# Kernel tuning notes

Hardware: AMD Instinct MI355X
Metric: run time of the kernel (lower is better)

Reference implementation:

```python
import jax, jax.numpy as jnp
import numpy as np

N_NODES = 100000
N_EDGES = 1600000
C_IN = 500
HIDDEN = 256
C_OUT = 50
K = 10
K_HALF = K // 2  # 5
ALPHA = 0.1


def _prop(x, src, dst, norm, n):
    # one propagate(): gather source features, scale by edge norm, scatter-add to dst
    msg = norm[:, None] * x[src]          # [E, F]
    return jax.ops.segment_sum(msg, dst, num_segments=n)


def setup_inputs() -> dict:
    key = jax.random.key(0)
    k0, k1, k2, k3 = jax.random.split(key, 4)
    x = jax.random.normal(k0, (N_NODES, C_IN), dtype=jnp.float32)
    edge_index = jax.random.randint(k1, (2, N_EDGES), 0, N_NODES, dtype=jnp.int32)
    # temp[k] = alpha * (1-alpha)^(2k), k = 0..K//2  (even-order PPR coefficients)
    temp = jnp.asarray(ALPHA * (1.0 - ALPHA) ** (2 * np.arange(K_HALF + 1)), dtype=jnp.float32)
    W1 = jax.random.normal(k2, (C_IN, HIDDEN), dtype=jnp.float32) / np.sqrt(C_IN).astype(np.float32)
    b1 = jnp.zeros((HIDDEN,), jnp.float32)
    W2 = jax.random.normal(k3, (HIDDEN, C_OUT), dtype=jnp.float32) / np.sqrt(HIDDEN).astype(np.float32)
    b2 = jnp.zeros((C_OUT,), jnp.float32)
    return {"x": x, "edge_index": edge_index, "W1": W1, "b1": b1, "W2": W2, "b2": b2, "temp": temp}


def reference(x, edge_index, W1, b1, W2, b2, temp):
    n = x.shape[0]
    src, dst = edge_index[0], edge_index[1]
    # sym-normalized adjacency A_hat = D^-1/2 A D^-1/2.
    # (get_laplacian 'sym' then add_self_loops(-norm, 1.0): the -1/+1 diagonal
    #  entries cancel under scatter-add, leaving exactly A_hat.)
    deg = jax.ops.segment_sum(jnp.ones_like(src, dtype=x.dtype), src, num_segments=n)
    dinv = jnp.where(deg > 0, jax.lax.rsqrt(jnp.maximum(deg, 1e-12)), 0.0)
    norm = dinv[src] * dinv[dst]          # [E]

    # MLP (dropout is identity in eval mode)
    h = jax.nn.relu(x @ W1 + b1)
    h = h @ W2 + b2                        # [N, C_OUT]

    hidden0 = h * temp[0]

    def body(k, carry):
        xk, hid = carry
        xk = _prop(xk, src, dst, norm, n)  # A_hat @ x
        xk = _prop(xk, src, dst, norm, n)  # A_hat^2 @ x
        hid = hid + temp[k + 1] * xk
        return (xk, hid)

    _, hidden = jax.lax.fori_loop(0, K_HALF, body, (h, hidden0))
    return jax.nn.log_softmax(hidden, axis=1)
```

## Files before the change

### kernel.cpp

```cpp
#include <hip/hip_runtime.h>

#define NN 100000
#define CIN 500
#define KPAD 512
#define HID 256
#define COUT 50
#define NPADOUT 64
#define FPAD 64

#define NBLK 256
#define CB 128
#define NC ((NN + CB - 1) / CB)
#define NCB (NC * NBLK)
#define NCB2 (2 * NCB)

typedef __attribute__((ext_vector_type(8))) short short8;
typedef __attribute__((ext_vector_type(4))) float f32x4;

static __device__ __forceinline__ unsigned short f2bf(float f) {
  union { float f; unsigned u; } v; v.f = f;
  unsigned r = (v.u + 0x7fffu + ((v.u >> 16) & 1u)) >> 16;
  return (unsigned short)r;
}

static __device__ __forceinline__ int slotAt(const int* __restrict__ incl,
                                             const int* __restrict__ bpre, int g) {
  return g ? incl[g - 1] + bpre[(g - 1) >> 10] : 0;
}


__launch_bounds__(256)
__global__ void k_p1(const int* __restrict__ src, const int* __restrict__ dst,
                     int* __restrict__ blk_cnt, int E, int chunk) {
  __shared__ int bd[NC], bs[NC];
  int tid = threadIdx.x;
  for (int i = tid; i < NC; i += 256) { bd[i] = 0; bs[i] = 0; }
  __syncthreads();
  int e0 = blockIdx.x * chunk, e1 = min(E, e0 + chunk);
  for (int e = e0 + tid; e < e1; e += 256) {
    atomicAdd(&bd[dst[e] >> 7], 1);
    atomicAdd(&bs[src[e] >> 7], 1);
  }
  __syncthreads();
  for (int i = tid; i < NC; i += 256) {
    blk_cnt[i * NBLK + blockIdx.x] = bd[i];
    blk_cnt[NCB + i * NBLK + blockIdx.x] = bs[i];
  }
}


__global__ void k_scan_a(const int* __restrict__ hist, int* __restrict__ incl,
                         int* __restrict__ bsum, int n) {
  __shared__ int ts[256];
  int tid = threadIdx.x;
  int base = blockIdx.x * 1024 + tid * 4;
  int a0 = 0, a1 = 0, a2 = 0, a3 = 0;
  if (base + 3 < n) {
    a0 = hist[base]; a1 = hist[base + 1]; a2 = hist[base + 2]; a3 = hist[base + 3];
  } else {
    if (base     < n) a0 = hist[base];
    if (base + 1 < n) a1 = hist[base + 1];
    if (base + 2 < n) a2 = hist[base + 2];
    if (base + 3 < n) a3 = hist[base + 3];
  }
  a1 += a0; a2 += a1; a3 += a2;
  ts[tid] = a3;
  __syncthreads();
  for (int o = 1; o < 256; o <<= 1) {
    int v = ts[tid];
    if (tid >= o) v += ts[tid - o];
    __syncthreads();
    ts[tid] = v;
    __syncthreads();
  }
  int ex = tid ? ts[tid - 1] : 0;
  if (base     < n) incl[base]     = a0 + ex;
  if (base + 1 < n) incl[base + 1] = a1 + ex;
  if (base + 2 < n) incl[base + 2] = a2 + ex;
  if (base + 3 < n) incl[base + 3] = a3 + ex;
  if (tid == 255) bsum[blockIdx.x] = ts[255];
}

__global__ void k_scan_b(const int* __restrict__ bsum, int* __restrict__ bpre, int nb) {
  __shared__ int s[512];
  int tid = threadIdx.x;
  s[tid] = (tid < nb) ? bsum[tid] : 0;
  __syncthreads();
  for (int o = 1; o < 512; o <<= 1) {
    int v = s[tid];
    if (tid >= o) v += s[tid - o];
    __syncthreads();
    s[tid] = v;
    __syncthreads();
  }
  if (tid < nb) bpre[tid] = tid ? s[tid - 1] : 0;
}


__launch_bounds__(256)
__global__ void k_p2(const int* __restrict__ src, const int* __restrict__ dst,
                     const int* __restrict__ incl, const int* __restrict__ bpre,
                     int* __restrict__ pkd, unsigned char* __restrict__ pks, int E, int chunk) {
  __shared__ int cd[NC], cs[NC];
  int tid = threadIdx.x;
  for (int i = tid; i < NC; i += 256) {
    cd[i] = slotAt(incl, bpre, i * NBLK + blockIdx.x);
    cs[i] = slotAt(incl, bpre, NCB + i * NBLK + blockIdx.x) - E;
  }
  __syncthreads();
  int e0 = blockIdx.x * chunk, e1 = min(E, e0 + chunk);
  for (int e = e0 + tid; e < e1; e += 256) {
    int s = src[e], d = dst[e];
    int pd = atomicAdd(&cd[d >> 7], 1);
    pkd[pd] = (s << 7) | (d & 127);
    int ps = atomicAdd(&cs[s >> 7], 1);
    pks[ps] = (unsigned char)(s & 127);
  }
}


__launch_bounds__(256)
__global__ void k_p3s(const int* __restrict__ incl, const int* __restrict__ bpre,
                      const unsigned char* __restrict__ pks, float* __restrict__ dinv, int E) {
  __shared__ int hist[CB];
  int b = blockIdx.x, tid = threadIdx.x;
  if (tid < CB) hist[tid] = 0;
  __syncthreads();
  int s0 = slotAt(incl, bpre, NCB + b * NBLK) - E;
  int s1 = slotAt(incl, bpre, NCB + (b + 1) * NBLK) - E;
  for (int e = s0 + tid; e < s1; e += 256) atomicAdd(&hist[pks[e]], 1);
  __syncthreads();
  if (tid < CB) {
    int node = b * CB + tid;
    if (node < NN) {
      int c = hist[tid];
      dinv[node] = c > 0 ? rsqrtf((float)c) : 0.f;
    }
  }
}


__launch_bounds__(256)
__global__ void k_p3d(const int* __restrict__ incl, const int* __restrict__ bpre,
                      const int* __restrict__ pkd, const float* __restrict__ dinv,
                      int* __restrict__ offs, int2* __restrict__ epk, int E) {
  __shared__ int hist[CB], base[CB], cur[CB];
  int b = blockIdx.x, tid = threadIdx.x;
  if (tid < CB) hist[tid] = 0;
  __syncthreads();
  int s0 = slotAt(incl, bpre, b * NBLK);
  int s1 = slotAt(incl, bpre, (b + 1) * NBLK);
  for (int e = s0 + tid; e < s1; e += 256) atomicAdd(&hist[pkd[e] & 127], 1);
  __syncthreads();
  if (tid == 0) {
    int acc = s0;
    for (int i = 0; i < CB; i++) { base[i] = acc; cur[i] = acc; acc += hist[i]; }
  }
  __syncthreads();
  if (tid < CB) {
    int node = b * CB + tid;
    if (node < NN) offs[node] = base[tid];
  }
  if (b == gridDim.x - 1 && tid == 0) offs[NN] = E;
  for (int e = s0 + tid; e < s1; e += 256) {
    int pk = pkd[e];
    int fine = pk & 127, s = pk >> 7;
    int pos = atomicAdd(&cur[fine], 1);
    float nm = dinv[s] * dinv[b * CB + fine];
    epk[pos] = make_int2(s, __float_as_int(nm));
  }
}


__global__ void k_wt(const float* __restrict__ W1, const float* __restrict__ W2,
                     unsigned short* __restrict__ W1T, unsigned short* __restrict__ W2T) {
  int idx = blockIdx.x * 256 + threadIdx.x;
  if (idx < HID * KPAD) {
    int n = idx >> 9, k = idx & 511;
    W1T[idx] = (k < CIN) ? f2bf(W1[(long)k * HID + n]) : (unsigned short)0;
  } else if (idx < HID * KPAD + NPADOUT * HID) {
    int i2 = idx - HID * KPAD;
    int n = i2 >> 8, k = i2 & 255;
    W2T[i2] = (n < COUT) ? f2bf(W2[(long)k * COUT + n]) : (unsigned short)0;
  }
}


#define LOADS(ra0_, ra1_, rb0_, rb1_, kkc)                                        \
  {                                                                               \
    const int kk_ = (kkc);                                                        \
    bool okk = kk_ + sc * 4 <= 496;                                               \
    if (okA && okk) ra0_ = *reinterpret_cast<const float4*>(&X[xbaseA + kk_]);    \
    else { ra0_.x = ra0_.y = ra0_.z = ra0_.w = 0.f; }                             \
    if (okB && okk) ra1_ = *reinterpret_cast<const float4*>(&X[xbaseB + kk_]);    \
    else { ra1_.x = ra1_.y = ra1_.z = ra1_.w = 0.f; }                             \
    rb0_ = *reinterpret_cast<const uint4*>(&W1T[wbase0 + kk_]);                   \
    rb1_ = *reinterpret_cast<const uint4*>(&W1T[wbase1 + kk_]);                   \
  }

#define STORE_LDS(As_, Bs_, ra0_, ra1_, rb0_, rb1_)                               \
  {                                                                               \
    ushort4 v0, v1;                                                               \
    v0.x = f2bf(ra0_.x); v0.y = f2bf(ra0_.y); v0.z = f2bf(ra0_.z); v0.w = f2bf(ra0_.w); \
    v1.x = f2bf(ra1_.x); v1.y = f2bf(ra1_.y); v1.z = f2bf(ra1_.z); v1.w = f2bf(ra1_.w); \
    *reinterpret_cast<ushort4*>(&As_[sr * 40 + sc * 4]) = v0;                     \
    *reinterpret_cast<ushort4*>(&As_[(sr + 64) * 40 + sc * 4]) = v1;              \
    *reinterpret_cast<uint4*>(&Bs_[br * 40 + bc * 8]) = rb0_;                     \
    *reinterpret_cast<uint4*>(&Bs_[(br + 128) * 40 + bc * 8]) = rb1_;             \
  }

#define COMPUTE(As_, Bs_)                                                         \
  {                                                                               \
    short8 af[4], bfr[4];                                                         \
    const int koff = (lane >> 4) * 8;                                             \
    _Pragma("unroll")                                                             \
    for (int i = 0; i < 4; i++)                                                   \
      af[i] = *reinterpret_cast<const short8*>(&As_[(wr * 64 + i * 16 + (lane & 15)) * 40 + koff]); \
    _Pragma("unroll")                                                             \
    for (int j = 0; j < 4; j++)                                                   \
      bfr[j] = *reinterpret_cast<const short8*>(&Bs_[(wc * 64 + j * 16 + (lane & 15)) * 40 + koff]); \
    _Pragma("unroll")                                                             \
    for (int i = 0; i < 4; i++)                                                   \
      _Pragma("unroll")                                                           \
      for (int j = 0; j < 4; j++)                                                 \
        acc[i][j] = __builtin_amdgcn_mfma_f32_16x16x32_bf16(af[i], bfr[j], acc[i][j], 0, 0, 0); \
  }

__launch_bounds__(512)
__global__ void k_mlp(const float* __restrict__ X, const unsigned short* __restrict__ W1T,
                      const float* __restrict__ b1, const unsigned short* __restrict__ W2T,
                      const float* __restrict__ b2, unsigned short* __restrict__ X0B) {
  __shared__ unsigned short smem[2 * 15360];
  const int tid = threadIdx.x;
  const int lane = tid & 63, w = tid >> 6;
  const int wr = w >> 2, wc = w & 3;
  const int row0 = blockIdx.x * 128;
  f32x4 acc[4][4] = {};
  const int sr = tid >> 3, sc = tid & 7;
  const int br = tid >> 2, bc = tid & 3;

  float4 raA0, raA1; uint4 rbA0, rbA1;
  float4 raB0, raB1; uint4 rbB0, rbB1;

  const int growA = row0 + sr;
  const int growB = row0 + sr + 64;
  const bool okA = growA < NN, okB = growB < NN;
  const long xbaseA = (long)growA * CIN + sc * 4;
  const long xbaseB = (long)growB * CIN + sc * 4;
  const long wbase0 = (long)br * KPAD + bc * 8;
  const long wbase1 = (long)(br + 128) * KPAD + bc * 8;

  LOADS(raA0, raA1, rbA0, rbA1, 0);
  LOADS(raB0, raB1, rbB0, rbB1, 32);

#pragma unroll
  for (int tt = 0; tt < 8; tt++) {
    const int kk0 = tt * 64;
    {
      unsigned short* As = smem;
      unsigned short* Bs = smem + 128 * 40;
      STORE_LDS(As, Bs, raA0, raA1, rbA0, rbA1);
      __syncthreads();
      if (kk0 + 64 < KPAD) LOADS(raA0, raA1, rbA0, rbA1, kk0 + 64);
      COMPUTE(As, Bs);
    }
    {
      unsigned short* As = smem + 15360;
      unsigned short* Bs = As + 128 * 40;
      STORE_LDS(As, Bs, raB0, raB1, rbB0, rbB1);
      __syncthreads();
      if (kk0 + 96 < KPAD) LOADS(raB0, raB1, rbB0, rbB1, kk0 + 96);
      COMPUTE(As, Bs);
    }
  }

  unsigned short* Hs = smem;
  const int rt = w >> 1;
  const int jh = w & 1;
#pragma unroll
  for (int ph = 0; ph < 2; ph++) {
    __syncthreads();
    if (wr == ph) {
#pragma unroll
      for (int i = 0; i < 4; i++) {
        int lr = i * 16 + (lane >> 4) * 4;
#pragma unroll
        for (int j = 0; j < 4; j++) {
          int col = wc * 64 + j * 16 + (lane & 15);
          float bv = b1[col];
#pragma unroll
          for (int r = 0; r < 4; r++) {
            float v = acc[i][j][r] + bv;
            v = v > 0.f ? v : 0.f;
            Hs[(lr + r) * 264 + col] = f2bf(v);
          }
        }
      }
    }
    __syncthreads();
    f32x4 acc2[2] = {};
    const int koff = (lane >> 4) * 8;
    for (int kk = 0; kk < HID; kk += 32) {
      short8 a = *reinterpret_cast<const short8*>(&Hs[(rt * 16 + (lane & 15)) * 264 + kk + koff]);
#pragma unroll
      for (int jj = 0; jj < 2; jj++) {
        int n = (jh * 2 + jj) * 16 + (lane & 15);
        short8 b = *reinterpret_cast<const short8*>(&W2T[n * HID + kk + koff]);
        acc2[jj] = __builtin_amdgcn_mfma_f32_16x16x32_bf16(a, b, acc2[jj], 0, 0, 0);
      }
    }
#pragma unroll
    for (int jj = 0; jj < 2; jj++) {
      int col = (jh * 2 + jj) * 16 + (lane & 15);
      float bv = (col < COUT) ? b2[col] : 0.f;
#pragma unroll
      for (int r = 0; r < 4; r++) {
        int row = row0 + ph * 64 + rt * 16 + (lane >> 4) * 4 + r;
        if (row < NN) {
          float v = acc2[jj][r] + bv;
          X0B[((long)row << 6) + col] = f2bf(v);
        }
      }
    }
  }
}


__launch_bounds__(256)
__global__ void k_prop(const int* __restrict__ offs, const int2* __restrict__ epk,
                       const unsigned short* __restrict__ xin,
                       unsigned short* __restrict__ xout) {
  const long long* __restrict__ epk8 = reinterpret_cast<const long long*>(epk);
  int node = blockIdx.x * 16 + (threadIdx.x >> 4);
  if (node >= NN) return;
  int h = threadIdx.x & 15;
  int fp = h * 4;
  int s0 = offs[node], s1 = offs[node + 1];
  float a0 = 0.f, a1 = 0.f, a2 = 0.f, a3 = 0.f;
  int e = s0;
  for (; e + 7 < s1; e += 8) {
    long long p[8];
#pragma unroll
    for (int q = 0; q < 8; q++) p[q] = epk8[e + q];
    uint2 v[8];
#pragma unroll
    for (int q = 0; q < 8; q++)
      v[q] = *reinterpret_cast<const uint2*>(&xin[((long)(int)p[q] << 6) + fp]);
#pragma unroll
    for (int q = 0; q < 8; q++) {
      float wq = __int_as_float((int)(p[q] >> 32));
      a0 += wq * __uint_as_float(v[q].x << 16);
      a1 += wq * __uint_as_float(v[q].x & 0xffff0000u);
      a2 += wq * __uint_as_float(v[q].y << 16);
      a3 += wq * __uint_as_float(v[q].y & 0xffff0000u);
    }
  }
  for (; e + 3 < s1; e += 4) {
    long long p0 = epk8[e], p1 = epk8[e + 1], p2 = epk8[e + 2], p3 = epk8[e + 3];
    uint2 v0 = *reinterpret_cast<const uint2*>(&xin[((long)(int)p0 << 6) + fp]);
    uint2 v1 = *reinterpret_cast<const uint2*>(&xin[((long)(int)p1 << 6) + fp]);
    uint2 v2 = *reinterpret_cast<const uint2*>(&xin[((long)(int)p2 << 6) + fp]);
    uint2 v3 = *reinterpret_cast<const uint2*>(&xin[((long)(int)p3 << 6) + fp]);
    float w0 = __int_as_float((int)(p0 >> 32)), w1 = __int_as_float((int)(p1 >> 32));
    float w2 = __int_as_float((int)(p2 >> 32)), w3 = __int_as_float((int)(p3 >> 32));
    a0 += w0 * __uint_as_float(v0.x << 16) + w1 * __uint_as_float(v1.x << 16)
        + w2 * __uint_as_float(v2.x << 16) + w3 * __uint_as_float(v3.x << 16);
    a1 += w0 * __uint_as_float(v0.x & 0xffff0000u) + w1 * __uint_as_float(v1.x & 0xffff0000u)
        + w2 * __uint_as_float(v2.x & 0xffff0000u) + w3 * __uint_as_float(v3.x & 0xffff0000u);
    a2 += w0 * __uint_as_float(v0.y << 16) + w1 * __uint_as_float(v1.y << 16)
        + w2 * __uint_as_float(v2.y << 16) + w3 * __uint_as_float(v3.y << 16);
    a3 += w0 * __uint_as_float(v0.y & 0xffff0000u) + w1 * __uint_as_float(v1.y & 0xffff0000u)
        + w2 * __uint_as_float(v2.y & 0xffff0000u) + w3 * __uint_as_float(v3.y & 0xffff0000u);
  }
  for (; e < s1; e++) {
    long long p0 = epk8[e];
    float w0 = __int_as_float((int)(p0 >> 32));
    uint2 v0 = *reinterpret_cast<const uint2*>(&xin[((long)(int)p0 << 6) + fp]);
    a0 += w0 * __uint_as_float(v0.x << 16);
    a1 += w0 * __uint_as_float(v0.x & 0xffff0000u);
    a2 += w0 * __uint_as_float(v0.y << 16);
    a3 += w0 * __uint_as_float(v0.y & 0xffff0000u);
  }
  unsigned d0 = ((unsigned)f2bf(a1) << 16) | (unsigned)f2bf(a0);
  unsigned d1 = ((unsigned)f2bf(a3) << 16) | (unsigned)f2bf(a2);
  unsigned long long pk8 = ((unsigned long long)d1 << 32) | d0;
  *reinterpret_cast<unsigned long long*>(&xout[((long)node << 6) + fp]) = pk8;
}


__launch_bounds__(256)
__global__ void k_fin(const unsigned short* __restrict__ x0,
                      const unsigned short* __restrict__ x1,
                      const unsigned short* __restrict__ x2,
                      const unsigned short* __restrict__ x3,
                      const unsigned short* __restrict__ x4,
                      const unsigned short* __restrict__ x5,
                      const float* __restrict__ temp, float* __restrict__ out) {
  int node = blockIdx.x * 4 + (threadIdx.x >> 6);
  if (node >= NN) return;
  int f = threadIdx.x & 63;
  float v = -INFINITY;
  if (f < COUT) {
    long idx = ((long)node << 6) + f;
    v = temp[0] * __uint_as_float((unsigned)x0[idx] << 16)
      + temp[1] * __uint_as_float((unsigned)x1[idx] << 16)
      + temp[2] * __uint_as_float((unsigned)x2[idx] << 16)
      + temp[3] * __uint_as_float((unsigned)x3[idx] << 16)
      + temp[4] * __uint_as_float((unsigned)x4[idx] << 16)
      + temp[5] * __uint_as_float((unsigned)x5[idx] << 16);
  }
  float m = v;
#pragma unroll
  for (int o = 32; o > 0; o >>= 1) m = fmaxf(m, __shfl_xor(m, o, 64));
  float ex = (f < COUT) ? expf(v - m) : 0.f;
  float s = ex;
#pragma unroll
  for (int o = 32; o > 0; o >>= 1) s += __shfl_xor(s, o, 64);
  if (f < COUT) out[(long)node * COUT + f] = (v - m) - logf(s);
}


extern "C" void kernel_launch(void* const* d_in, const int* in_sizes, int n_in,
                              void* d_out, int out_size, void* d_ws, size_t ws_size,
                              hipStream_t stream) {
  const float* X  = (const float*)d_in[0];
  const int* EI   = (const int*)d_in[1];
  const float* W1 = (const float*)d_in[2];
  const float* B1 = (const float*)d_in[3];
  const float* W2 = (const float*)d_in[4];
  const float* B2 = (const float*)d_in[5];
  const float* TEMP = (const float*)d_in[6];
  const int E = in_sizes[1] / 2;
  const int* src = EI;
  const int* dst = EI + E;

  char* ws = (char*)d_ws;
  size_t off = 0;
  auto alloc = [&](size_t bytes) -> void* {
    off = (off + 511) & ~(size_t)511;
    void* p = ws + off;
    off += bytes;
    return p;
  };
  unsigned short* W1T = (unsigned short*)alloc((size_t)HID * KPAD * 2);
  unsigned short* W2T = (unsigned short*)alloc((size_t)NPADOUT * HID * 2);
  unsigned short* XB[7];
  for (int i = 0; i < 7; i++) XB[i] = (unsigned short*)alloc((size_t)NN * FPAD * 2);
  float* DINV = (float*)alloc((size_t)NN * 4);
  int* OFFS   = (int*)alloc((size_t)(NN + 1) * 4);
  int* BLKC   = (int*)alloc((size_t)NCB2 * 4);
  int* INCL   = (int*)alloc((size_t)NCB2 * 4);
  int* BSUM   = (int*)alloc(512 * 4);
  int* BPRE   = (int*)alloc(512 * 4);
  int* PKD    = (int*)alloc((size_t)E * 4);
  unsigned char* PKS = (unsigned char*)alloc((size_t)E);
  int2* EPK   = (int2*)alloc((size_t)E * 8);

  const int chunk = (E + NBLK - 1) / NBLK;
  const int nsa = (NCB2 + 1023) / 1024;

  k_p1<<<NBLK, 256, 0, stream>>>(src, dst, BLKC, E, chunk);
  k_scan_a<<<nsa, 256, 0, stream>>>(BLKC, INCL, BSUM, NCB2);
  k_scan_b<<<1, 512, 0, stream>>>(BSUM, BPRE, nsa);
  k_p2<<<NBLK, 256, 0, stream>>>(src, dst, INCL, BPRE, PKD, PKS, E, chunk);
  k_p3s<<<NC, 256, 0, stream>>>(INCL, BPRE, PKS, DINV, E);
  k_p3d<<<NC, 256, 0, stream>>>(INCL, BPRE, PKD, DINV, OFFS, EPK, E);

  k_wt<<<(HID * KPAD + NPADOUT * HID + 255) / 256, 256, 0, stream>>>(W1, W2, W1T, W2T);

  k_mlp<<<(NN + 127) / 128, 512, 0, stream>>>(X, W1T, B1, W2T, B2, XB[0]);

  const int PB = (NN + 15) / 16;
  for (int k = 0; k < 5; k++) {
    k_prop<<<PB, 256, 0, stream>>>(OFFS, EPK, XB[k], XB[6]);
    k_prop<<<PB, 256, 0, stream>>>(OFFS, EPK, XB[6], XB[k + 1]);
  }
  k_fin<<<(NN + 3) / 4, 256, 0, stream>>>(XB[0], XB[1], XB[2], XB[3], XB[4], XB[5],
                                          TEMP, (float*)d_out);
}
```

Before: 790.5 us.

## Pre-convert X to padded bf16 and stream MLP tiles via global_load_lds

Adds a conversion kernel that writes X as a zero-padded bf16 matrix (512 columns, padded rows), then a new MLP kernel that loads A and W1 tiles straight into LDS with global_load_lds before doing MFMA. The goal is to halve the bytes the GEMM reads and drop the register-staged fp32 loads, conversion and LDS stores from the GEMM inner loop. The cost is an extra ~100 MB write and read pass plus workspace space. The new LDS layout has no padding, so LDS bank conflicts are possible. It falls back to the old kernel when the workspace is too small.

```diff
diff --git a/kernel.cpp b/kernel.cpp
--- a/kernel.cpp
+++ b/kernel.cpp
@@ -1,6 +1,7 @@
 #include <hip/hip_runtime.h>
 
 #define NN 100000
+#define NROWP 100096
 #define CIN 500
 #define KPAD 512
 #define HID 256
@@ -182,6 +183,129 @@
     int i2 = idx - HID * KPAD;
     int n = i2 >> 8, k = i2 & 255;
     W2T[i2] = (n < COUT) ? f2bf(W2[(long)k * COUT + n]) : (unsigned short)0;
+  }
+}
+
+
+__launch_bounds__(256)
+__global__ void k_cvt(const float* __restrict__ X, unsigned short* __restrict__ XC) {
+  const long total = (long)NROWP * KPAD;
+  long idx = ((long)blockIdx.x * 256 + threadIdx.x) * 8;
+  const long stride = (long)gridDim.x * 256 * 8;
+  for (; idx < total; idx += stride) {
+    int row = (int)(idx >> 9);
+    int c = (int)(idx & 511);
+    ushort4 o0 = {0, 0, 0, 0}, o1 = {0, 0, 0, 0};
+    if (row < NN && c < CIN) {
+      const float* xp = &X[(long)row * CIN + c];
+      if (c + 8 <= CIN) {
+        float4 f0 = *reinterpret_cast<const float4*>(xp);
+        float4 f1 = *reinterpret_cast<const float4*>(xp + 4);
+        o0.x = f2bf(f0.x); o0.y = f2bf(f0.y); o0.z = f2bf(f0.z); o0.w = f2bf(f0.w);
+        o1.x = f2bf(f1.x); o1.y = f2bf(f1.y); o1.z = f2bf(f1.z); o1.w = f2bf(f1.w);
+      } else {
+        o0.x = f2bf(xp[0]); o0.y = f2bf(xp[1]); o0.z = f2bf(xp[2]); o0.w = f2bf(xp[3]);
+      }
+    }
+    *reinterpret_cast<ushort4*>(&XC[idx]) = o0;
+    *reinterpret_cast<ushort4*>(&XC[idx + 4]) = o1;
+  }
+}
+
+
+__launch_bounds__(512)
+__global__ void k_mlp_lds(const unsigned short* __restrict__ XC,
+                          const unsigned short* __restrict__ W1T,
+                          const float* __restrict__ b1,
+                          const unsigned short* __restrict__ W2T,
+                          const float* __restrict__ b2,
+                          unsigned short* __restrict__ X0B) {
+  __shared__ unsigned short smem[64 * 264];
+  const int tid = threadIdx.x;
+  const int lane = tid & 63, w = tid >> 6;
+  const int wr = w >> 2, wc = w & 3;
+  const int row0 = blockIdx.x * 128;
+  f32x4 acc[4][4] = {};
+
+  const int l2 = lane >> 2, l3 = lane & 3;
+  const unsigned short* gA  = XC  + (((long)(row0 + 16 * w + l2)) << 9) + l3 * 8;
+  const unsigned short* gB0 = W1T + (((long)(32 * w + l2)) << 9) + l3 * 8;
+  const unsigned short* gB1 = W1T + (((long)(32 * w + 16 + l2)) << 9) + l3 * 8;
+  unsigned short* ldsA  = smem + w * 512;
+  unsigned short* ldsB0 = smem + 4096 + 2 * w * 512;
+  unsigned short* ldsB1 = smem + 4096 + (2 * w + 1) * 512;
+
+  for (int kk = 0; kk < KPAD; kk += 32) {
+    __syncthreads();
+    __builtin_amdgcn_global_load_lds((const void*)(gA + kk),  (void*)ldsA,  16, 0, 0);
+    __builtin_amdgcn_global_load_lds((const void*)(gB0 + kk), (void*)ldsB0, 16, 0, 0);
+    __builtin_amdgcn_global_load_lds((const void*)(gB1 + kk), (void*)ldsB1, 16, 0, 0);
+    __syncthreads();
+    short8 af[4], bfr[4];
+    const int koff = (lane >> 4) * 8;
+#pragma unroll
+    for (int i = 0; i < 4; i++)
+      af[i] = *reinterpret_cast<const short8*>(
+          &smem[(wr * 64 + i * 16 + (lane & 15)) * 32 + koff]);
+#pragma unroll
+    for (int j = 0; j < 4; j++)
+      bfr[j] = *reinterpret_cast<const short8*>(
+          &smem[4096 + (wc * 64 + j * 16 + (lane & 15)) * 32 + koff]);
+#pragma unroll
+    for (int i = 0; i < 4; i++)
+#pragma unroll
+      for (int j = 0; j < 4; j++)
+        acc[i][j] = __builtin_amdgcn_mfma_f32_16x16x32_bf16(af[i], bfr[j], acc[i][j], 0, 0, 0);
+  }
+
+  unsigned short* Hs = smem;
+  const int rt = w >> 1;
+  const int jh = w & 1;
+#pragma unroll
+  for (int ph = 0; ph < 2; ph++) {
+    __syncthreads();
+    if (wr == ph) {
+#pragma unroll
+      for (int i = 0; i < 4; i++) {
+        int lr = i * 16 + (lane >> 4) * 4;
+#pragma unroll
+        for (int j = 0; j < 4; j++) {
+          int col = wc * 64 + j * 16 + (lane & 15);
+          float bv = b1[col];
+#pragma unroll
+          for (int r = 0; r < 4; r++) {
+            float v = acc[i][j][r] + bv;
+            v = v > 0.f ? v : 0.f;
+            Hs[(lr + r) * 264 + col] = f2bf(v);
+          }
+        }
+      }
+    }
+    __syncthreads();
+    f32x4 acc2[2] = {};
+    const int koff = (lane >> 4) * 8;
+    for (int kk = 0; kk < HID; kk += 32) {
+      short8 a = *reinterpret_cast<const short8*>(&Hs[(rt * 16 + (lane & 15)) * 264 + kk + koff]);
+#pragma unroll
+      for (int jj = 0; jj < 2; jj++) {
+        int n = (jh * 2 + jj) * 16 + (lane & 15);
+        short8 b = *reinterpret_cast<const short8*>(&W2T[n * HID + kk + koff]);
+        acc2[jj] = __builtin_amdgcn_mfma_f32_16x16x32_bf16(a, b, acc2[jj], 0, 0, 0);
+      }
+    }
+#pragma unroll
+    for (int jj = 0; jj < 2; jj++) {
+      int col = (jh * 2 + jj) * 16 + (lane & 15);
+      float bv = (col < COUT) ? b2[col] : 0.f;
+#pragma unroll
+      for (int r = 0; r < 4; r++) {
+        int row = row0 + ph * 64 + rt * 16 + (lane >> 4) * 4 + r;
+        if (row < NN) {
+          float v = acc2[jj][r] + bv;
+          X0B[((long)row << 6) + col] = f2bf(v);
+        }
+      }
+    }
   }
 }
 
@@ -456,6 +580,13 @@
   unsigned char* PKS = (unsigned char*)alloc((size_t)E);
   int2* EPK   = (int2*)alloc((size_t)E * 8);
 
+  const size_t xc_bytes = (size_t)NROWP * KPAD * 2;
+  unsigned short* XC = nullptr;
+  {
+    size_t need = ((off + 511) & ~(size_t)511) + xc_bytes;
+    if (need <= ws_size) XC = (unsigned short*)alloc(xc_bytes);
+  }
+
   const int chunk = (E + NBLK - 1) / NBLK;
   const int nsa = (NCB2 + 1023) / 1024;
 
@@ -468,7 +599,12 @@
 
   k_wt<<<(HID * KPAD + NPADOUT * HID + 255) / 256, 256, 0, stream>>>(W1, W2, W1T, W2T);
 
-  k_mlp<<<(NN + 127) / 128, 512, 0, stream>>>(X, W1T, B1, W2T, B2, XB[0]);
+  if (XC) {
+    k_cvt<<<2048, 256, 0, stream>>>(X, XC);
+    k_mlp_lds<<<(NN + 127) / 128, 512, 0, stream>>>(XC, W1T, B1, W2T, B2, XB[0]);
+  } else {
+    k_mlp<<<(NN + 127) / 128, 512, 0, stream>>>(X, W1T, B1, W2T, B2, XB[0]);
+  }
 
   const int PB = (NN + 15) / 16;
   for (int k = 0; k < 5; k++) {
```

Measured after the change: 844.5 us. +6.8%, slower.
